# Performance work log

Measured on AMD Instinct MI355X. Metric: run time of the kernel, lower is better.

## Reference

```python
import jax, jax.numpy as jnp
import numpy as np

D_MODEL = 1024
NUM_HEADS = 16
DFF = 4096
LN_EPS = 1e-08
CLIP = 10.0


def setup_inputs() -> dict:
    key = jax.random.key(0)
    ks = jax.random.split(key, 12)
    d, h, f = D_MODEL, NUM_HEADS, DFF
    s = 1.0 / np.sqrt(d)
    inp = {
        "x": jax.random.normal(ks[0], (4, 2048, d), dtype=jnp.float32),
        "wq": jax.random.normal(ks[1], (d, d), dtype=jnp.float32) * s,
        "bq": jnp.zeros((d,), jnp.float32),
        "wk": jax.random.normal(ks[2], (d, d), dtype=jnp.float32) * s,
        "bk": jnp.zeros((d,), jnp.float32),
        "wv": jax.random.normal(ks[3], (d, d), dtype=jnp.float32) * s,
        "bv": jnp.zeros((d,), jnp.float32),
        "wo": jax.random.normal(ks[4], (d, d), dtype=jnp.float32) * s,
        "bo": jnp.zeros((d,), jnp.float32),
        "w1": jax.random.normal(ks[5], (d, f), dtype=jnp.float32) * s,
        "b1": jnp.zeros((f,), jnp.float32),
        "w2": jax.random.normal(ks[6], (f, d), dtype=jnp.float32) * (1.0 / np.sqrt(f)),
        "b2": jnp.zeros((d,), jnp.float32),
        "ln_gamma": jnp.ones((d,), jnp.float32),
        "ln_beta": jnp.zeros((d,), jnp.float32),
    }
    return inp


def layernorm(x, gamma, beta):
    mu = jnp.mean(x, axis=-1, keepdims=True)
    var = jnp.var(x, axis=-1, keepdims=True)
    return (x - mu) * jax.lax.rsqrt(var + LN_EPS) * gamma + beta


def encoder_layer(x, wq, bq, wk, bk, wv, bv, wo, bo, w1, b1, w2, b2, ln_gamma, ln_beta):
    B, S, d = x.shape
    H = NUM_HEADS
    Dh = d // H
    q = (x @ wq + bq).reshape(B, S, H, Dh).transpose(0, 2, 1, 3)  # bhsd
    k = (x @ wk + bk).reshape(B, S, H, Dh).transpose(0, 2, 1, 3)
    v = (x @ wv + bv).reshape(B, S, H, Dh).transpose(0, 2, 1, 3)
    logits = jnp.einsum('bhqd,bhkd->bhqk', q, k) / jnp.sqrt(jnp.float32(Dh))
    logits = jnp.clip(logits, -CLIP, CLIP)
    attn = jax.nn.softmax(logits, axis=-1)
    ctx = jnp.einsum('bhqk,bhkd->bhqd', attn, v)
    ctx = ctx.transpose(0, 2, 1, 3).reshape(B, S, d)
    attn_out = ctx @ wo + bo
    out1 = layernorm(x + attn_out, ln_gamma, ln_beta)
    ffn = jax.nn.relu(out1 @ w1 + b1) @ w2 + b2
    return layernorm(out1 + ffn, ln_gamma, ln_beta)


def reference(x, wq, bq, wk, bk, wv, bv, wo, bo, w1, b1, w2, b2, ln_gamma, ln_beta):
    return encoder_layer(x, wq, bq, wk, bk, wv, bv, wo, bo, w1, b1, w2, b2, ln_gamma, ln_beta)
```

## Files before the change

kernel.cpp:

```cpp
#include <hip/hip_runtime.h>
#include <stdint.h>

#define D_MODEL 1024
#define NHEAD 16
#define DH 64
#define DFF 4096
#define BATCH 4
#define SEQ 2048
#define MTOT (BATCH*SEQ)

typedef short short8 __attribute__((ext_vector_type(8)));
typedef float f32x4 __attribute__((ext_vector_type(4)));
typedef unsigned int uint;

__device__ inline unsigned short f2bf(float f) {
  union { float f; unsigned u; } v; v.f = f;
  unsigned r = v.u + 0x7fffu + ((v.u >> 16) & 1u);
  return (unsigned short)(r >> 16);
}
__device__ inline float bf2f(unsigned short b) {
  union { unsigned u; float f; } v; v.u = ((unsigned)b) << 16;
  return v.f;
}
__device__ inline unsigned pack_trunc(float lo, float hi) {
  union { float f; unsigned u; } a, b; a.f = lo; b.f = hi;
  return __builtin_amdgcn_perm(b.u, a.u, 0x07060302u);
}
__device__ __forceinline__ void async16(const unsigned short* g, unsigned short* l) {
  __builtin_amdgcn_global_load_lds(
      (const __attribute__((address_space(1))) unsigned int*)g,
      (__attribute__((address_space(3))) unsigned int*)l, 16, 0, 0);
}

__global__ void cast_kernel(const float* __restrict__ in, unsigned short* __restrict__ out, int n4) {
  int i = blockIdx.x * blockDim.x + threadIdx.x;
  if (i < n4) {
    float4 v = ((const float4*)in)[i];
    ushort4 o;
    o.x = f2bf(v.x); o.y = f2bf(v.y); o.z = f2bf(v.z); o.w = f2bf(v.w);
    ((ushort4*)out)[i] = o;
  }
}

__global__ void transpose_cast_kernel(const float* __restrict__ in, unsigned short* __restrict__ out,
                                      int K, int N, float scale) {
  __shared__ unsigned short tile[32][33];
  int n0 = blockIdx.x * 32, k0 = blockIdx.y * 32;
  int tx = threadIdx.x & 31, ty = threadIdx.x >> 5;
#pragma unroll
  for (int j = 0; j < 32; j += 8)
    tile[ty + j][tx] = f2bf(in[(size_t)(k0 + ty + j) * N + n0 + tx] * scale);
  __syncthreads();
#pragma unroll
  for (int j = 0; j < 32; j += 8)
    out[(size_t)(n0 + ty + j) * K + k0 + tx] = tile[tx][ty + j];
}

__global__ void bias_concat_kernel(const float* __restrict__ bq, const float* __restrict__ bk,
                                   const float* __restrict__ bv, float* __restrict__ o) {
  int i = blockIdx.x * 256 + threadIdx.x;
  if (i < 3 * D_MODEL) {
    float v = (i < D_MODEL) ? bq[i] * 0.125f
            : (i < 2 * D_MODEL) ? bk[i - D_MODEL] : bv[i - 2 * D_MODEL];
    o[i] = v;
  }
}

__global__ void transpose_v_kernel(const unsigned short* __restrict__ QKV,
                                   unsigned short* __restrict__ Vt) {
  __shared__ unsigned short tile[32][33];
  int bh = blockIdx.z, b = bh >> 4, h = bh & 15;
  int kv0 = blockIdx.x * 32, dh0 = blockIdx.y * 32;
  int tx = threadIdx.x & 31, ty = threadIdx.x >> 5;
#pragma unroll
  for (int j = 0; j < 32; j += 8)
    tile[ty + j][tx] = QKV[(size_t)(b * SEQ + kv0 + ty + j) * 3072 + 2048 + h * DH + dh0 + tx];
  __syncthreads();
#pragma unroll
  for (int j = 0; j < 32; j += 8)
    Vt[(size_t)(bh * DH + dh0 + ty + j) * SEQ + kv0 + tx] = tile[tx][ty + j];
}

template<int RELU, int OUT_BF16>
__global__ __launch_bounds__(256, 2) void gemm_bt_kernel(
    const unsigned short* __restrict__ A,
    const unsigned short* __restrict__ Bt,
    const float* __restrict__ bias,
    void* __restrict__ Cout,
    int M, int N, int K) {
  __shared__ __align__(16) unsigned short As[128][32];
  __shared__ __align__(16) unsigned short Bs[128][32];
  const int GX = N >> 7;
  const int xcd = blockIdx.x & 7;
  const int li = blockIdx.x >> 3;
  const int im = xcd * 8 + li / GX;
  const int in_ = li % GX;
  const int m0 = im * 128, n0 = in_ * 128;
  const int tid = threadIdx.x;
  const int wave = tid >> 6, lane = tid & 63;
  const int wm = (wave >> 1) * 64, wn = (wave & 1) * 64;
  const int lm = lane & 15, lq = lane >> 4, lk = (lane >> 4) * 8;
  const int sr = tid >> 2;
  const int sc = (tid & 3) * 8;
  f32x4 acc[4][4] = {};

  for (int k0 = 0; k0 < K; k0 += 32) {
    __syncthreads();
#pragma unroll
    for (int s = 0; s < 2; s++) {
      int row = sr + s * 64;
      async16(A  + (size_t)(m0 + row) * K + k0 + sc, &As[0][0] + row * 32 + sc);
      async16(Bt + (size_t)(n0 + row) * K + k0 + sc, &Bs[0][0] + row * 32 + sc);
    }
    __syncthreads();
    short8 af[4], bfr[4];
#pragma unroll
    for (int t = 0; t < 4; t++) {
      af[t]  = *(const short8*)(&As[wm + t * 16 + lm][lk]);
      bfr[t] = *(const short8*)(&Bs[wn + t * 16 + lm][lk]);
    }
#pragma unroll
    for (int mt = 0; mt < 4; mt++)
#pragma unroll
      for (int nt = 0; nt < 4; nt++)
        acc[mt][nt] = __builtin_amdgcn_mfma_f32_16x16x32_bf16(af[mt], bfr[nt], acc[mt][nt], 0, 0, 0);
  }
#pragma unroll
  for (int nt = 0; nt < 4; nt++) {
    int col = n0 + wn + nt * 16 + lm;
    float bv = bias[col];
#pragma unroll
    for (int mt = 0; mt < 4; mt++) {
#pragma unroll
      for (int r = 0; r < 4; r++) {
        int row = m0 + wm + mt * 16 + lq * 4 + r;
        float v = acc[mt][nt][r] + bv;
        if (RELU) v = fmaxf(v, 0.0f);
        if (OUT_BF16) ((unsigned short*)Cout)[(size_t)row * N + col] = f2bf(v);
        else          ((float*)Cout)[(size_t)row * N + col] = v;
      }
    }
  }
}

__global__ __launch_bounds__(256, 4) void attn_kernel(
    const unsigned short* __restrict__ QKV,
    const unsigned short* __restrict__ Vt_g,
    unsigned short* __restrict__ ctx) {
  __shared__ __align__(16) unsigned short Ks[64 * 64];
  __shared__ __align__(16) unsigned short Vs[64 * 64];
  __shared__ __align__(16) unsigned short Ps[4 * 32 * 64];
  const int bh = blockIdx.x, b = bh >> 4, h = bh & 15;
  const int q0 = blockIdx.y * 128;
  const int tid = threadIdx.x, wave = tid >> 6, lane = tid & 63;
  const int lm = lane & 15, lq = lane >> 4;
  const int srow = tid >> 3, scol = (tid & 7) * 8;

  short8 qf[2][2];
#pragma unroll
  for (int ntq = 0; ntq < 2; ntq++) {
    const unsigned short* qp = QKV + (size_t)(b * SEQ + q0 + wave * 32 + ntq * 16 + lm) * 3072 + h * DH;
#pragma unroll
    for (int sl = 0; sl < 2; sl++) qf[ntq][sl] = *(const short8*)(qp + sl * 32 + lq * 8);
  }
  const short8 ones = {0x3F80, 0x3F80, 0x3F80, 0x3F80, 0x3F80, 0x3F80, 0x3F80, 0x3F80};
  f32x4 oacc[2][4] = {};
  f32x4 lsum[2] = {};

  const int sdst = srow * 64 + (scol ^ ((srow & 7) * 8));
  const unsigned short* kg = QKV + (size_t)(b * SEQ) * 3072 + D_MODEL + h * DH + scol;
  const unsigned short* vg = Vt_g + (size_t)(bh * DH + srow) * SEQ + scol;
  const int rot = (lm & 7) * 8;

  for (int kv0 = 0; kv0 < SEQ; kv0 += 64) {
    __syncthreads();
    *(uint4*)(Ks + sdst)        = *(const uint4*)(kg + (size_t)(kv0 + srow) * 3072);
    *(uint4*)(Ks + sdst + 2048) = *(const uint4*)(kg + (size_t)(kv0 + srow + 32) * 3072);
    *(uint4*)(Vs + sdst)        = *(const uint4*)(vg + kv0);
    *(uint4*)(Vs + sdst + 2048) = *(const uint4*)(vg + 32 * SEQ + kv0);
    __syncthreads();

#pragma unroll
    for (int mt = 0; mt < 4; mt++) {
      const unsigned short* krow = Ks + (mt * 16 + lm) * 64;
      short8 kf0 = *(const short8*)(krow + ((lq * 8) ^ rot));
      short8 kf1 = *(const short8*)(krow + ((32 + lq * 8) ^ rot));
#pragma unroll
      for (int ntq = 0; ntq < 2; ntq++) {
        f32x4 sa = {0.f, 0.f, 0.f, 0.f};
        sa = __builtin_amdgcn_mfma_f32_16x16x32_bf16(kf0, qf[ntq][0], sa, 0, 0, 0);
        sa = __builtin_amdgcn_mfma_f32_16x16x32_bf16(kf1, qf[ntq][1], sa, 0, 0, 0);
        float p0 = __expf(fminf(sa[0], 10.0f));
        float p1 = __expf(fminf(sa[1], 10.0f));
        float p2 = __expf(fminf(sa[2], 10.0f));
        float p3 = __expf(fminf(sa[3], 10.0f));
        uint2 d;
        d.x = pack_trunc(p0, p1);
        d.y = pack_trunc(p2, p3);
        *(uint2*)(Ps + wave * 2048 + (ntq * 16 + lm) * 64 + ((mt * 16 + lq * 4) ^ rot)) = d;
      }
    }
    __builtin_amdgcn_s_waitcnt(0xC07F);
    short8 pf[2][2];
#pragma unroll
    for (int mq = 0; mq < 2; mq++)
#pragma unroll
      for (int sl = 0; sl < 2; sl++)
        pf[mq][sl] = *(const short8*)(Ps + wave * 2048 + (mq * 16 + lm) * 64 + ((sl * 32 + lq * 8) ^ rot));
#pragma unroll
    for (int nt = 0; nt < 4; nt++) {
      const unsigned short* vrow = Vs + (nt * 16 + lm) * 64;
      short8 vf0 = *(const short8*)(vrow + ((lq * 8) ^ rot));
      short8 vf1 = *(const short8*)(vrow + ((32 + lq * 8) ^ rot));
#pragma unroll
      for (int mq = 0; mq < 2; mq++) {
        oacc[mq][nt] = __builtin_amdgcn_mfma_f32_16x16x32_bf16(pf[mq][0], vf0, oacc[mq][nt], 0, 0, 0);
        oacc[mq][nt] = __builtin_amdgcn_mfma_f32_16x16x32_bf16(pf[mq][1], vf1, oacc[mq][nt], 0, 0, 0);
      }
    }
#pragma unroll
    for (int mq = 0; mq < 2; mq++) {
      lsum[mq] = __builtin_amdgcn_mfma_f32_16x16x32_bf16(pf[mq][0], ones, lsum[mq], 0, 0, 0);
      lsum[mq] = __builtin_amdgcn_mfma_f32_16x16x32_bf16(pf[mq][1], ones, lsum[mq], 0, 0, 0);
    }
  }

#pragma unroll
  for (int mq = 0; mq < 2; mq++) {
    float linv[4];
#pragma unroll
    for (int r = 0; r < 4; r++) linv[r] = 1.0f / lsum[mq][r];
    const size_t rowbase = (size_t)(b * SEQ + q0 + wave * 32 + mq * 16 + lq * 4) * D_MODEL + h * DH;
#pragma unroll
    for (int nt = 0; nt < 4; nt++) {
#pragma unroll
      for (int r = 0; r < 4; r++) {
        ctx[rowbase + (size_t)r * D_MODEL + nt * 16 + lm] = f2bf(oacc[mq][nt][r] * linv[r]);
      }
    }
  }
}

template<int B_BF16, int WRITE_BF16>
__global__ void ln_kernel(const float* __restrict__ A, const void* __restrict__ Bv,
                          const float* __restrict__ gamma, const float* __restrict__ beta,
                          float* __restrict__ outf, unsigned short* __restrict__ outb) {
  const int row = blockIdx.x;
  const int tid = threadIdx.x;
  const size_t base = (size_t)row * D_MODEL + tid * 4;
  float4 xa = *(const float4*)(A + base);
  float4 xb;
  if (B_BF16) {
    ushort4 u = *(const ushort4*)((const unsigned short*)Bv + base);
    xb.x = bf2f(u.x); xb.y = bf2f(u.y); xb.z = bf2f(u.z); xb.w = bf2f(u.w);
  } else {
    xb = *(const float4*)((const float*)Bv + base);
  }
  float v0 = xa.x + xb.x, v1 = xa.y + xb.y, v2 = xa.z + xb.z, v3 = xa.w + xb.w;
  float s = v0 + v1 + v2 + v3;
  float sq = v0 * v0 + v1 * v1 + v2 * v2 + v3 * v3;
#pragma unroll
  for (int off = 1; off < 64; off <<= 1) {
    s  += __shfl_xor(s, off);
    sq += __shfl_xor(sq, off);
  }
  __shared__ float red[8];
  int wave = tid >> 6;
  if ((tid & 63) == 0) { red[wave * 2] = s; red[wave * 2 + 1] = sq; }
  __syncthreads();
  s  = red[0] + red[2] + red[4] + red[6];
  sq = red[1] + red[3] + red[5] + red[7];
  float mean = s * (1.0f / D_MODEL);
  float var = sq * (1.0f / D_MODEL) - mean * mean;
  float inv = rsqrtf(var + 1e-8f);
  float4 g  = *(const float4*)(gamma + tid * 4);
  float4 be = *(const float4*)(beta + tid * 4);
  float o0 = (v0 - mean) * inv * g.x + be.x;
  float o1 = (v1 - mean) * inv * g.y + be.y;
  float o2 = (v2 - mean) * inv * g.z + be.z;
  float o3 = (v3 - mean) * inv * g.w + be.w;
  float4 of; of.x = o0; of.y = o1; of.z = o2; of.w = o3;
  *(float4*)(outf + base) = of;
  if (WRITE_BF16) {
    ushort4 ub; ub.x = f2bf(o0); ub.y = f2bf(o1); ub.z = f2bf(o2); ub.w = f2bf(o3);
    *(ushort4*)(outb + base) = ub;
  }
}

extern "C" void kernel_launch(void* const* d_in, const int* in_sizes, int n_in,
                              void* d_out, int out_size, void* d_ws, size_t ws_size,
                              hipStream_t stream) {
  const float* x     = (const float*)d_in[0];
  const float* wq    = (const float*)d_in[1];
  const float* bq    = (const float*)d_in[2];
  const float* wk    = (const float*)d_in[3];
  const float* bk    = (const float*)d_in[4];
  const float* wv    = (const float*)d_in[5];
  const float* bv    = (const float*)d_in[6];
  const float* wo    = (const float*)d_in[7];
  const float* bo    = (const float*)d_in[8];
  const float* w1    = (const float*)d_in[9];
  const float* b1    = (const float*)d_in[10];
  const float* w2    = (const float*)d_in[11];
  const float* b2    = (const float*)d_in[12];
  const float* gamma = (const float*)d_in[13];
  const float* beta  = (const float*)d_in[14];

  char* ws = (char*)d_ws;
  const size_t MB = 1ull << 20;
  unsigned short* xb      = (unsigned short*)(ws + 0 * MB);
  unsigned short* out1b   = (unsigned short*)(ws + 0 * MB);
  unsigned short* wqkvT   = (unsigned short*)(ws + 16 * MB);
  unsigned short* woT     = (unsigned short*)(ws + 22 * MB);
  unsigned short* w1T     = (unsigned short*)(ws + 24 * MB);
  unsigned short* w2T     = (unsigned short*)(ws + 32 * MB);
  float*          bqkv    = (float*)(ws + 40 * MB);
  unsigned short* qkvb    = (unsigned short*)(ws + 41 * MB);
  unsigned short* attnoutb= (unsigned short*)(ws + 41 * MB);
  unsigned short* h1      = (unsigned short*)(ws + 41 * MB);
  unsigned short* Vt_g    = (unsigned short*)(ws + 89 * MB);
  unsigned short* ctx     = (unsigned short*)(ws + 105 * MB);
  unsigned short* ffnb    = (unsigned short*)(ws + 105 * MB);
  float*          out1f   = (float*)(ws + 121 * MB);

  cast_kernel<<<(MTOT * D_MODEL / 4 + 255) / 256, 256, 0, stream>>>(x, xb, MTOT * D_MODEL / 4);
  transpose_cast_kernel<<<dim3(32, 32), 256, 0, stream>>>(wq, wqkvT, D_MODEL, D_MODEL, 0.125f);
  transpose_cast_kernel<<<dim3(32, 32), 256, 0, stream>>>(wk, wqkvT + 1024 * 1024, D_MODEL, D_MODEL, 1.0f);
  transpose_cast_kernel<<<dim3(32, 32), 256, 0, stream>>>(wv, wqkvT + 2 * 1024 * 1024, D_MODEL, D_MODEL, 1.0f);
  transpose_cast_kernel<<<dim3(32, 32), 256, 0, stream>>>(wo, woT, D_MODEL, D_MODEL, 1.0f);
  transpose_cast_kernel<<<dim3(128, 32), 256, 0, stream>>>(w1, w1T, D_MODEL, DFF, 1.0f);
  transpose_cast_kernel<<<dim3(32, 128), 256, 0, stream>>>(w2, w2T, DFF, D_MODEL, 1.0f);
  bias_concat_kernel<<<12, 256, 0, stream>>>(bq, bk, bv, bqkv);

  gemm_bt_kernel<0, 1><<<(3072 / 128) * (MTOT / 128), 256, 0, stream>>>(
      xb, wqkvT, bqkv, qkvb, MTOT, 3072, D_MODEL);
  transpose_v_kernel<<<dim3(SEQ / 32, DH / 32, BATCH * NHEAD), 256, 0, stream>>>(qkvb, Vt_g);
  attn_kernel<<<dim3(BATCH * NHEAD, SEQ / 128), 256, 0, stream>>>(qkvb, Vt_g, ctx);

  gemm_bt_kernel<0, 1><<<(D_MODEL / 128) * (MTOT / 128), 256, 0, stream>>>(
      ctx, woT, bo, attnoutb, MTOT, D_MODEL, D_MODEL);
  ln_kernel<1, 1><<<MTOT, 256, 0, stream>>>(x, attnoutb, gamma, beta, out1f, out1b);
  gemm_bt_kernel<1, 1><<<(DFF / 128) * (MTOT / 128), 256, 0, stream>>>(
      out1b, w1T, b1, h1, MTOT, DFF, D_MODEL);
  gemm_bt_kernel<0, 1><<<(D_MODEL / 128) * (MTOT / 128), 256, 0, stream>>>(
      h1, w2T, b2, ffnb, MTOT, D_MODEL, DFF);
  ln_kernel<1, 0><<<MTOT, 256, 0, stream>>>(out1f, ffnb, gamma, beta, (float*)d_out, nullptr);
}
```

Before: 568.0 us.

## Double-buffer K/V tiles and double query rows per attention block

The attention kernel now prefetches the next K/V tile into registers while computing on the current one, using double-buffered shared memory so only one barrier per iteration is needed. Each wave now handles 64 query rows instead of 32, halving the grid and the number of times K/V are loaded per query. The cost is higher register and LDS use, with launch bounds lowered to 2 blocks per CU, which cuts occupancy. The grid also shrinks to 512 blocks, which could leave some CUs idle.

Measured after the change: 548.2 us. 3.5% less time.

```diff
diff --git a/kernel.cpp b/kernel.cpp
--- a/kernel.cpp
+++ b/kernel.cpp
@@ -143,53 +143,68 @@
   }
 }
 
-__global__ __launch_bounds__(256, 4) void attn_kernel(
+__global__ __launch_bounds__(256, 2) void attn_kernel(
     const unsigned short* __restrict__ QKV,
     const unsigned short* __restrict__ Vt_g,
     unsigned short* __restrict__ ctx) {
-  __shared__ __align__(16) unsigned short Ks[64 * 64];
-  __shared__ __align__(16) unsigned short Vs[64 * 64];
-  __shared__ __align__(16) unsigned short Ps[4 * 32 * 64];
+  __shared__ __align__(16) unsigned short Ks[2][64 * 64];
+  __shared__ __align__(16) unsigned short Vs[2][64 * 64];
+  __shared__ __align__(16) unsigned short Ps[4][64 * 64];
   const int bh = blockIdx.x, b = bh >> 4, h = bh & 15;
-  const int q0 = blockIdx.y * 128;
+  const int q0 = blockIdx.y * 256;
   const int tid = threadIdx.x, wave = tid >> 6, lane = tid & 63;
   const int lm = lane & 15, lq = lane >> 4;
   const int srow = tid >> 3, scol = (tid & 7) * 8;
-
-  short8 qf[2][2];
-#pragma unroll
-  for (int ntq = 0; ntq < 2; ntq++) {
-    const unsigned short* qp = QKV + (size_t)(b * SEQ + q0 + wave * 32 + ntq * 16 + lm) * 3072 + h * DH;
-#pragma unroll
-    for (int sl = 0; sl < 2; sl++) qf[ntq][sl] = *(const short8*)(qp + sl * 32 + lq * 8);
+  const int rot = (lm & 7) * 8;
+
+  short8 qf[4][2];
+#pragma unroll
+  for (int qt = 0; qt < 4; qt++) {
+    const unsigned short* qp =
+        QKV + (size_t)(b * SEQ + q0 + wave * 64 + qt * 16 + lm) * 3072 + h * DH;
+#pragma unroll
+    for (int sl = 0; sl < 2; sl++) qf[qt][sl] = *(const short8*)(qp + sl * 32 + lq * 8);
   }
   const short8 ones = {0x3F80, 0x3F80, 0x3F80, 0x3F80, 0x3F80, 0x3F80, 0x3F80, 0x3F80};
-  f32x4 oacc[2][4] = {};
-  f32x4 lsum[2] = {};
+  f32x4 oacc[4][4] = {};
+  f32x4 lsum[4] = {};
 
   const int sdst = srow * 64 + (scol ^ ((srow & 7) * 8));
   const unsigned short* kg = QKV + (size_t)(b * SEQ) * 3072 + D_MODEL + h * DH + scol;
   const unsigned short* vg = Vt_g + (size_t)(bh * DH + srow) * SEQ + scol;
-  const int rot = (lm & 7) * 8;
-
-  for (int kv0 = 0; kv0 < SEQ; kv0 += 64) {
+
+  uint4 kr0 = *(const uint4*)(kg + (size_t)srow * 3072);
+  uint4 kr1 = *(const uint4*)(kg + (size_t)(srow + 32) * 3072);
+  uint4 vr0 = *(const uint4*)(vg);
+  uint4 vr1 = *(const uint4*)(vg + 32 * SEQ);
+
+  for (int it = 0; it < SEQ / 64; it++) {
+    unsigned short* ks = Ks[it & 1];
+    unsigned short* vs = Vs[it & 1];
+    *(uint4*)(ks + sdst)        = kr0;
+    *(uint4*)(ks + sdst + 2048) = kr1;
+    *(uint4*)(vs + sdst)        = vr0;
+    *(uint4*)(vs + sdst + 2048) = vr1;
     __syncthreads();
-    *(uint4*)(Ks + sdst)        = *(const uint4*)(kg + (size_t)(kv0 + srow) * 3072);
-    *(uint4*)(Ks + sdst + 2048) = *(const uint4*)(kg + (size_t)(kv0 + srow + 32) * 3072);
-    *(uint4*)(Vs + sdst)        = *(const uint4*)(vg + kv0);
-    *(uint4*)(Vs + sdst + 2048) = *(const uint4*)(vg + 32 * SEQ + kv0);
-    __syncthreads();
-
+    if (it + 1 < SEQ / 64) {
+      const int kvn = (it + 1) * 64;
+      kr0 = *(const uint4*)(kg + (size_t)(kvn + srow) * 3072);
+      kr1 = *(const uint4*)(kg + (size_t)(kvn + srow + 32) * 3072);
+      vr0 = *(const uint4*)(vg + kvn);
+      vr1 = *(const uint4*)(vg + 32 * SEQ + kvn);
+    }
+
+    unsigned short* ps = Ps[wave];
 #pragma unroll
     for (int mt = 0; mt < 4; mt++) {
-      const unsigned short* krow = Ks + (mt * 16 + lm) * 64;
+      const unsigned short* krow = ks + (mt * 16 + lm) * 64;
       short8 kf0 = *(const short8*)(krow + ((lq * 8) ^ rot));
       short8 kf1 = *(const short8*)(krow + ((32 + lq * 8) ^ rot));
 #pragma unroll
-      for (int ntq = 0; ntq < 2; ntq++) {
+      for (int qt = 0; qt < 4; qt++) {
         f32x4 sa = {0.f, 0.f, 0.f, 0.f};
-        sa = __builtin_amdgcn_mfma_f32_16x16x32_bf16(kf0, qf[ntq][0], sa, 0, 0, 0);
-        sa = __builtin_amdgcn_mfma_f32_16x16x32_bf16(kf1, qf[ntq][1], sa, 0, 0, 0);
+        sa = __builtin_amdgcn_mfma_f32_16x16x32_bf16(kf0, qf[qt][0], sa, 0, 0, 0);
+        sa = __builtin_amdgcn_mfma_f32_16x16x32_bf16(kf1, qf[qt][1], sa, 0, 0, 0);
         float p0 = __expf(fminf(sa[0], 10.0f));
         float p1 = __expf(fminf(sa[1], 10.0f));
         float p2 = __expf(fminf(sa[2], 10.0f));
@@ -197,45 +212,46 @@
         uint2 d;
         d.x = pack_trunc(p0, p1);
         d.y = pack_trunc(p2, p3);
-        *(uint2*)(Ps + wave * 2048 + (ntq * 16 + lm) * 64 + ((mt * 16 + lq * 4) ^ rot)) = d;
+        *(uint2*)(ps + (qt * 16 + lm) * 64 + ((mt * 16 + lq * 4) ^ rot)) = d;
       }
     }
     __builtin_amdgcn_s_waitcnt(0xC07F);
-    short8 pf[2][2];
-#pragma unroll
-    for (int mq = 0; mq < 2; mq++)
+    short8 pf[4][2];
+#pragma unroll
+    for (int qt = 0; qt < 4; qt++)
 #pragma unroll
       for (int sl = 0; sl < 2; sl++)
-        pf[mq][sl] = *(const short8*)(Ps + wave * 2048 + (mq * 16 + lm) * 64 + ((sl * 32 + lq * 8) ^ rot));
+        pf[qt][sl] = *(const short8*)(ps + (qt * 16 + lm) * 64 + ((sl * 32 + lq * 8) ^ rot));
 #pragma unroll
     for (int nt = 0; nt < 4; nt++) {
-      const unsigned short* vrow = Vs + (nt * 16 + lm) * 64;
+      const unsigned short* vrow = vs + (nt * 16 + lm) * 64;
       short8 vf0 = *(const short8*)(vrow + ((lq * 8) ^ rot));
       short8 vf1 = *(const short8*)(vrow + ((32 + lq * 8) ^ rot));
 #pragma unroll
-      for (int mq = 0; mq < 2; mq++) {
-        oacc[mq][nt] = __builtin_amdgcn_mfma_f32_16x16x32_bf16(pf[mq][0], vf0, oacc[mq][nt], 0, 0, 0);
-        oacc[mq][nt] = __builtin_amdgcn_mfma_f32_16x16x32_bf16(pf[mq][1], vf1, oacc[mq][nt], 0, 0, 0);
+      for (int qt = 0; qt < 4; qt++) {
+        oacc[qt][nt] = __builtin_amdgcn_mfma_f32_16x16x32_bf16(pf[qt][0], vf0, oacc[qt][nt], 0, 0, 0);
+        oacc[qt][nt] = __builtin_amdgcn_mfma_f32_16x16x32_bf16(pf[qt][1], vf1, oacc[qt][nt], 0, 0, 0);
       }
     }
 #pragma unroll
-    for (int mq = 0; mq < 2; mq++) {
-      lsum[mq] = __builtin_amdgcn_mfma_f32_16x16x32_bf16(pf[mq][0], ones, lsum[mq], 0, 0, 0);
-      lsum[mq] = __builtin_amdgcn_mfma_f32_16x16x32_bf16(pf[mq][1], ones, lsum[mq], 0, 0, 0);
-    }
-  }
-
-#pragma unroll
-  for (int mq = 0; mq < 2; mq++) {
+    for (int qt = 0; qt < 4; qt++) {
+      lsum[qt] = __builtin_amdgcn_mfma_f32_16x16x32_bf16(pf[qt][0], ones, lsum[qt], 0, 0, 0);
+      lsum[qt] = __builtin_amdgcn_mfma_f32_16x16x32_bf16(pf[qt][1], ones, lsum[qt], 0, 0, 0);
+    }
+  }
+
+#pragma unroll
+  for (int qt = 0; qt < 4; qt++) {
     float linv[4];
 #pragma unroll
-    for (int r = 0; r < 4; r++) linv[r] = 1.0f / lsum[mq][r];
-    const size_t rowbase = (size_t)(b * SEQ + q0 + wave * 32 + mq * 16 + lq * 4) * D_MODEL + h * DH;
+    for (int r = 0; r < 4; r++) linv[r] = 1.0f / lsum[qt][r];
+    const size_t rowbase =
+        (size_t)(b * SEQ + q0 + wave * 64 + qt * 16 + lq * 4) * D_MODEL + h * DH;
 #pragma unroll
     for (int nt = 0; nt < 4; nt++) {
 #pragma unroll
       for (int r = 0; r < 4; r++) {
-        ctx[rowbase + (size_t)r * D_MODEL + nt * 16 + lm] = f2bf(oacc[mq][nt][r] * linv[r]);
+        ctx[rowbase + (size_t)r * D_MODEL + nt * 16 + lm] = f2bf(oacc[qt][nt][r] * linv[r]);
       }
     }
   }
@@ -335,7 +351,7 @@
   gemm_bt_kernel<0, 1><<<(3072 / 128) * (MTOT / 128), 256, 0, stream>>>(
       xb, wqkvT, bqkv, qkvb, MTOT, 3072, D_MODEL);
   transpose_v_kernel<<<dim3(SEQ / 32, DH / 32, BATCH * NHEAD), 256, 0, stream>>>(qkvb, Vt_g);
-  attn_kernel<<<dim3(BATCH * NHEAD, SEQ / 128), 256, 0, stream>>>(qkvb, Vt_g, ctx);
+  attn_kernel<<<dim3(BATCH * NHEAD, SEQ / 256), 256, 0, stream>>>(qkvb, Vt_g, ctx);
 
   gemm_bt_kernel<0, 1><<<(D_MODEL / 128) * (MTOT / 128), 256, 0, stream>>>(
       ctx, woT, bo, attnoutb, MTOT, D_MODEL, D_MODEL);
```

## Prefetch K/V tiles into registers, use exp2 softmax, merge weight transposes

Applied to the files above, without the earlier changes.

The attention loop now loads the next K/V tile from global memory into registers while the current tile is being computed. This overlaps global latency with the MFMA work but adds register pressure. Q scaling folds in log2(e) so the softmax can use a native exp2 with a rescaled clip bound. The six weight transpose launches are merged into one launch with a 128x128x6 grid, and blocks outside each matrix exit early, trading fewer launches for many idle blocks.

New measurement: 568.0 us. Within noise of the previous version (-0.0%).

```diff
diff --git a/kernel.cpp b/kernel.cpp
--- a/kernel.cpp
+++ b/kernel.cpp
@@ -9,9 +9,18 @@
 #define SEQ 2048
 #define MTOT (BATCH*SEQ)
 
+#define QSCALE 0.18033688011112043f
+#define CLIP2  14.426950408889634f
+
 typedef short short8 __attribute__((ext_vector_type(8)));
 typedef float f32x4 __attribute__((ext_vector_type(4)));
 typedef unsigned int uint;
+
+#if __has_builtin(__builtin_amdgcn_exp2f)
+#define EXP2(x) __builtin_amdgcn_exp2f(x)
+#else
+#define EXP2(x) __expf((x) * 0.6931471805599453f)
+#endif
 
 __device__ inline unsigned short f2bf(float f) {
   union { float f; unsigned u; } v; v.f = f;
@@ -42,10 +51,24 @@
   }
 }
 
-__global__ void transpose_cast_kernel(const float* __restrict__ in, unsigned short* __restrict__ out,
-                                      int K, int N, float scale) {
+__global__ void transpose_weights_kernel(
+    const float* __restrict__ wq, const float* __restrict__ wk,
+    const float* __restrict__ wv, const float* __restrict__ wo,
+    const float* __restrict__ w1, const float* __restrict__ w2,
+    unsigned short* __restrict__ wqkvT, unsigned short* __restrict__ woT,
+    unsigned short* __restrict__ w1T, unsigned short* __restrict__ w2T) {
   __shared__ unsigned short tile[32][33];
+  const float* in; unsigned short* out; int K, N; float scale = 1.0f;
+  switch (blockIdx.z) {
+    case 0:  in = wq; out = wqkvT;           K = 1024; N = 1024; scale = QSCALE; break;
+    case 1:  in = wk; out = wqkvT + 1048576; K = 1024; N = 1024; break;
+    case 2:  in = wv; out = wqkvT + 2097152; K = 1024; N = 1024; break;
+    case 3:  in = wo; out = woT;             K = 1024; N = 1024; break;
+    case 4:  in = w1; out = w1T;             K = 1024; N = 4096; break;
+    default: in = w2; out = w2T;             K = 4096; N = 1024; break;
+  }
   int n0 = blockIdx.x * 32, k0 = blockIdx.y * 32;
+  if (n0 >= N || k0 >= K) return;
   int tx = threadIdx.x & 31, ty = threadIdx.x >> 5;
 #pragma unroll
   for (int j = 0; j < 32; j += 8)
@@ -60,7 +83,7 @@
                                    const float* __restrict__ bv, float* __restrict__ o) {
   int i = blockIdx.x * 256 + threadIdx.x;
   if (i < 3 * D_MODEL) {
-    float v = (i < D_MODEL) ? bq[i] * 0.125f
+    float v = (i < D_MODEL) ? bq[i] * QSCALE
             : (i < 2 * D_MODEL) ? bk[i - D_MODEL] : bv[i - 2 * D_MODEL];
     o[i] = v;
   }
@@ -155,11 +178,13 @@
   const int tid = threadIdx.x, wave = tid >> 6, lane = tid & 63;
   const int lm = lane & 15, lq = lane >> 4;
   const int srow = tid >> 3, scol = (tid & 7) * 8;
+  const int rot = (lm & 7) * 8;
 
   short8 qf[2][2];
 #pragma unroll
   for (int ntq = 0; ntq < 2; ntq++) {
-    const unsigned short* qp = QKV + (size_t)(b * SEQ + q0 + wave * 32 + ntq * 16 + lm) * 3072 + h * DH;
+    const unsigned short* qp =
+        QKV + (size_t)(b * SEQ + q0 + wave * 32 + ntq * 16 + lm) * 3072 + h * DH;
 #pragma unroll
     for (int sl = 0; sl < 2; sl++) qf[ntq][sl] = *(const short8*)(qp + sl * 32 + lq * 8);
   }
@@ -170,15 +195,25 @@
   const int sdst = srow * 64 + (scol ^ ((srow & 7) * 8));
   const unsigned short* kg = QKV + (size_t)(b * SEQ) * 3072 + D_MODEL + h * DH + scol;
   const unsigned short* vg = Vt_g + (size_t)(bh * DH + srow) * SEQ + scol;
-  const int rot = (lm & 7) * 8;
-
-  for (int kv0 = 0; kv0 < SEQ; kv0 += 64) {
+
+  uint4 kr0 = *(const uint4*)(kg + (size_t)srow * 3072);
+  uint4 kr1 = *(const uint4*)(kg + (size_t)(srow + 32) * 3072);
+  uint4 vr0 = *(const uint4*)(vg);
+  uint4 vr1 = *(const uint4*)(vg + 32 * SEQ);
+
+  for (int it = 0; it < SEQ / 64; it++) {
+    *(uint4*)(Ks + sdst)        = kr0;
+    *(uint4*)(Ks + sdst + 2048) = kr1;
+    *(uint4*)(Vs + sdst)        = vr0;
+    *(uint4*)(Vs + sdst + 2048) = vr1;
     __syncthreads();
-    *(uint4*)(Ks + sdst)        = *(const uint4*)(kg + (size_t)(kv0 + srow) * 3072);
-    *(uint4*)(Ks + sdst + 2048) = *(const uint4*)(kg + (size_t)(kv0 + srow + 32) * 3072);
-    *(uint4*)(Vs + sdst)        = *(const uint4*)(vg + kv0);
-    *(uint4*)(Vs + sdst + 2048) = *(const uint4*)(vg + 32 * SEQ + kv0);
-    __syncthreads();
+    if (it + 1 < SEQ / 64) {
+      const int kvn = (it + 1) * 64;
+      kr0 = *(const uint4*)(kg + (size_t)(kvn + srow) * 3072);
+      kr1 = *(const uint4*)(kg + (size_t)(kvn + srow + 32) * 3072);
+      vr0 = *(const uint4*)(vg + kvn);
+      vr1 = *(const uint4*)(vg + 32 * SEQ + kvn);
+    }
 
 #pragma unroll
     for (int mt = 0; mt < 4; mt++) {
@@ -190,10 +225,10 @@
         f32x4 sa = {0.f, 0.f, 0.f, 0.f};
         sa = __builtin_amdgcn_mfma_f32_16x16x32_bf16(kf0, qf[ntq][0], sa, 0, 0, 0);
         sa = __builtin_amdgcn_mfma_f32_16x16x32_bf16(kf1, qf[ntq][1], sa, 0, 0, 0);
-        float p0 = __expf(fminf(sa[0], 10.0f));
-        float p1 = __expf(fminf(sa[1], 10.0f));
-        float p2 = __expf(fminf(sa[2], 10.0f));
-        float p3 = __expf(fminf(sa[3], 10.0f));
+        float p0 = EXP2(fminf(sa[0], CLIP2));
+        float p1 = EXP2(fminf(sa[1], CLIP2));
+        float p2 = EXP2(fminf(sa[2], CLIP2));
+        float p3 = EXP2(fminf(sa[3], CLIP2));
         uint2 d;
         d.x = pack_trunc(p0, p1);
         d.y = pack_trunc(p2, p3);
@@ -223,6 +258,7 @@
       lsum[mq] = __builtin_amdgcn_mfma_f32_16x16x32_bf16(pf[mq][0], ones, lsum[mq], 0, 0, 0);
       lsum[mq] = __builtin_amdgcn_mfma_f32_16x16x32_bf16(pf[mq][1], ones, lsum[mq], 0, 0, 0);
     }
+    __syncthreads();
   }
 
 #pragma unroll
@@ -230,7 +266,8 @@
     float linv[4];
 #pragma unroll
     for (int r = 0; r < 4; r++) linv[r] = 1.0f / lsum[mq][r];
-    const size_t rowbase = (size_t)(b * SEQ + q0 + wave * 32 + mq * 16 + lq * 4) * D_MODEL + h * DH;
+    const size_t rowbase =
+        (size_t)(b * SEQ + q0 + wave * 32 + mq * 16 + lq * 4) * D_MODEL + h * DH;
 #pragma unroll
     for (int nt = 0; nt < 4; nt++) {
 #pragma unroll
@@ -324,12 +361,8 @@
   float*          out1f   = (float*)(ws + 121 * MB);
 
   cast_kernel<<<(MTOT * D_MODEL / 4 + 255) / 256, 256, 0, stream>>>(x, xb, MTOT * D_MODEL / 4);
-  transpose_cast_kernel<<<dim3(32, 32), 256, 0, stream>>>(wq, wqkvT, D_MODEL, D_MODEL, 0.125f);
-  transpose_cast_kernel<<<dim3(32, 32), 256, 0, stream>>>(wk, wqkvT + 1024 * 1024, D_MODEL, D_MODEL, 1.0f);
-  transpose_cast_kernel<<<dim3(32, 32), 256, 0, stream>>>(wv, wqkvT + 2 * 1024 * 1024, D_MODEL, D_MODEL, 1.0f);
-  transpose_cast_kernel<<<dim3(32, 32), 256, 0, stream>>>(wo, woT, D_MODEL, D_MODEL, 1.0f);
-  transpose_cast_kernel<<<dim3(128, 32), 256, 0, stream>>>(w1, w1T, D_MODEL, DFF, 1.0f);
-  transpose_cast_kernel<<<dim3(32, 128), 256, 0, stream>>>(w2, w2T, DFF, D_MODEL, 1.0f);
+  transpose_weights_kernel<<<dim3(128, 128, 6), 256, 0, stream>>>(
+      wq, wk, wv, wo, w1, w2, wqkvT, woT, w1T, w2T);
   bias_concat_kernel<<<12, 256, 0, stream>>>(bq, bk, bv, bqkv);
 
   gemm_bt_kernel<0, 1><<<(3072 / 128) * (MTOT / 128), 256, 0, stream>>>(
```
